# Kernel optimization log

Hardware: AMD Instinct MI355X
Metric: run time of the kernel (lower is better)

## Reference

```python
import jax, jax.numpy as jnp
import numpy as np

MARGIN = 0.3
NORM_EPS = 1e-12  # torch F.normalize default eps


def setup_inputs() -> dict:
    key = jax.random.key(0)
    k1, k2 = jax.random.split(key)
    embeddings = jax.random.normal(k1, (8192, 128), dtype=jnp.float32)
    labels = jax.random.randint(k2, (8192,), 0, 128, dtype=jnp.int64)
    return {"embeddings": embeddings, "labels": labels}


def _triplet_loss(embeddings, labels):
    # L2-normalize rows (torch F.normalize: x / max(||x||, eps))
    norm = jnp.linalg.norm(embeddings, axis=1, keepdims=True)
    e = embeddings / jnp.maximum(norm, NORM_EPS)

    # pairwise squared Euclidean via gram matrix
    dot = e @ e.T                     # [B, B]
    sq = jnp.diagonal(dot)            # [B]
    d2 = jnp.clip(sq[None, :] - 2.0 * dot + sq[:, None], 0.0)
    zmask = (d2 == 0.0).astype(d2.dtype)
    dist = jnp.sqrt(d2 + zmask * 1e-16) * (1.0 - zmask)  # [B, B]

    # hard mining, fully vectorized over rows
    same = labels[:, None] == labels[None, :]
    eye = jnp.eye(labels.shape[0], dtype=bool)
    pos_mask = same & ~eye
    neg_mask = ~same

    dist_ap = jnp.max(jnp.where(pos_mask, dist, -jnp.inf), axis=1)  # hardest positive
    dist_an = jnp.min(jnp.where(neg_mask, dist, jnp.inf), axis=1)   # hardest negative

    valid = pos_mask.any(axis=1) & neg_mask.any(axis=1)
    # MarginRankingLoss(margin)(dist_an, dist_ap, y=1) = mean relu(dist_ap - dist_an + margin)
    per_row = jnp.maximum(dist_ap - dist_an + MARGIN, 0.0)
    n_valid = jnp.maximum(jnp.sum(valid), 1).astype(dist.dtype)
    loss = jnp.sum(jnp.where(valid, per_row, 0.0)) / n_valid
    return jnp.where(valid.any(), loss, jnp.zeros((), dist.dtype))


def reference(embeddings, labels):
    return _triplet_loss(embeddings, labels)
```

## Files before the change

### kernel.cpp

```cpp
#include <hip/hip_runtime.h>
#include <cmath>

#define BN 8192
#define DIM 128
#define MARGIN_F 0.3f
#define NSPLIT 8
#define CPS 1024
#define NT 8
#define NPART (NSPLIT * 2)
#define FBLK 32
#define IMAX 0x7FFFFFFF
#define IMIN 0x80000000

typedef __attribute__((ext_vector_type(4))) int i32x4;

__device__ __forceinline__ int imin3(int a, int b, int c) { return min(a, min(b, c)); }
__device__ __forceinline__ int imax3(int a, int b, int c) { return max(a, max(b, c)); }

__global__ __launch_bounds__(256) void norm_cvt_k(
    const float* __restrict__ emb, float* __restrict__ sqv, unsigned short* __restrict__ EnQ16)
{
  int w = (blockIdx.x * blockDim.x + threadIdx.x) >> 6;
  int lane = threadIdx.x & 63;
  if (w >= BN) return;
  float2 v = *reinterpret_cast<const float2*>(&emb[w * DIM + lane * 2]);
  float s = v.x * v.x + v.y * v.y;
  #pragma unroll
  for (int off = 32; off > 0; off >>= 1) s += __shfl_xor(s, off);
  float iv = 1.0f / fmaxf(sqrtf(s), 1e-12f);
  if (lane == 0) sqv[w] = s * iv * iv;
  int q0 = (int)rintf(127.0f * v.x * iv);
  int q1 = (int)rintf(127.0f * v.y * iv);
  unsigned short us = (unsigned short)((q0 & 255) | ((q1 & 255) << 8));
  int g = lane >> 3;
  EnQ16[(g * BN + w) * 8 + (lane & 7)] = us;
}

__global__ __launch_bounds__(256, 2) void gram_mine_mfma_k(
    const char* __restrict__ EnQ, const int* __restrict__ lab,
    int* __restrict__ ap_part, int* __restrict__ an_part)
{
  __shared__ __align__(16) char Bs[2][16384];

  const int tid = threadIdx.x;
  const int w = tid >> 6, l = tid & 63;
  const int wr = w >> 1, wc = w & 1;
  const int lrow = l & 15, lkg = l >> 4;

  const int rowBase = blockIdx.x * 128 + wr * 64;
  const int panel   = blockIdx.y * CPS;

  i32x4 a[4][2];
  #pragma unroll
  for (int mi = 0; mi < 4; ++mi)
    #pragma unroll
    for (int kk = 0; kk < 2; ++kk)
      a[mi][kk] = *reinterpret_cast<const i32x4*>(
          EnQ + (((size_t)((kk << 2) + lkg) * BN + rowBase + mi * 16 + lrow) << 4));

  unsigned rlbp[4];
  #pragma unroll
  for (int mi = 0; mi < 4; ++mi) {
    int rb = rowBase + mi * 16 + lkg * 4;
    rlbp[mi] = (unsigned)(lab[rb] & 255) | ((unsigned)(lab[rb + 1] & 255) << 8) |
               ((unsigned)(lab[rb + 2] & 255) << 16) | ((unsigned)(lab[rb + 3] & 255) << 24);
  }

  int ap[4][4], an[4][4];
  #pragma unroll
  for (int mi = 0; mi < 4; ++mi)
    #pragma unroll
    for (int r = 0; r < 4; ++r) { ap[mi][r] = IMAX; an[mi][r] = IMIN; }

  auto stage = [&](int buf, int colTile) {
    #pragma unroll
    for (int i = 0; i < 4; ++i) {
      int s0 = (w << 8) + (i << 6);
      int s  = s0 + l;
      const char* gp = EnQ + (((size_t)(s >> 7) * BN + colTile + (s & 127)) << 4);
      __builtin_amdgcn_global_load_lds(
          (const __attribute__((address_space(1))) void*)gp,
          (__attribute__((address_space(3))) void*)(&Bs[buf][s0 * 16]),
          16, 0, 0);
    }
  };

  stage(0, panel);
  __syncthreads();

  int cur = 0;
  #pragma unroll 1
  for (int ct = 0; ct < NT; ++ct) {
    const int colTile = panel + ct * 128;
    const int colBase = colTile + wc * 64;

    if (ct + 1 < NT) stage(cur ^ 1, colTile + 128);

    int clb[4];
    #pragma unroll
    for (int ni = 0; ni < 4; ++ni) clb[ni] = lab[colBase + ni * 16 + lrow];

    const bool diag = (rowBase == colBase);

    #pragma unroll
    for (int half = 0; half < 2; ++half) {
      const int n0 = half * 2, n1 = half * 2 + 1;

      i32x4 acc[4][2] = {};
      #pragma unroll
      for (int kk = 0; kk < 2; ++kk) {
        i32x4 b[2];
        #pragma unroll
        for (int n = 0; n < 2; ++n)
          b[n] = *reinterpret_cast<const i32x4*>(
              &Bs[cur][(((kk << 2) + lkg) * 128 + wc * 64 + (n0 + n) * 16 + lrow) * 16]);
        #pragma unroll
        for (int mi = 0; mi < 4; ++mi)
          #pragma unroll
          for (int n = 0; n < 2; ++n)
            acc[mi][n] = __builtin_amdgcn_mfma_i32_16x16x64_i8(
                a[mi][kk], b[n], acc[mi][n], 0, 0, 0);
      }

      if (diag) {
        #pragma unroll
        for (int mi = 0; mi < 4; ++mi)
          #pragma unroll
          for (int r = 0; r < 4; ++r) {
            int rl = (int)((rlbp[mi] >> (r * 8)) & 255u);
            int rloc = mi * 16 + lkg * 4 + r;
            int d0 = acc[mi][0][r], d1 = acc[mi][1][r];
            bool s0 = (rl == clb[n0]), s1 = (rl == clb[n1]);
            bool e0 = (rloc == n0 * 16 + lrow), e1 = (rloc == n1 * 16 + lrow);
            int p0 = (s0 && !e0) ? d0 : IMAX;
            int p1 = (s1 && !e1) ? d1 : IMAX;
            int q0 = s0 ? IMIN : d0;
            int q1 = s1 ? IMIN : d1;
            ap[mi][r] = imin3(ap[mi][r], p0, p1);
            an[mi][r] = imax3(an[mi][r], q0, q1);
          }
      } else {
        #pragma unroll
        for (int mi = 0; mi < 4; ++mi)
          #pragma unroll
          for (int r = 0; r < 4; ++r) {
            int rl = (int)((rlbp[mi] >> (r * 8)) & 255u);
            int d0 = acc[mi][0][r], d1 = acc[mi][1][r];
            bool s0 = (rl == clb[n0]), s1 = (rl == clb[n1]);
            int p0 = s0 ? d0 : IMAX;
            int p1 = s1 ? d1 : IMAX;
            int q0 = s0 ? IMIN : d0;
            int q1 = s1 ? IMIN : d1;
            ap[mi][r] = imin3(ap[mi][r], p0, p1);
            an[mi][r] = imax3(an[mi][r], q0, q1);
          }
      }
    }

    __syncthreads();
    cur ^= 1;
  }

  const int part = blockIdx.y * 2 + wc;
  #pragma unroll
  for (int mi = 0; mi < 4; ++mi)
    #pragma unroll
    for (int r = 0; r < 4; ++r) {
      int p = ap[mi][r], n = an[mi][r];
      #pragma unroll
      for (int off = 1; off < 16; off <<= 1) {
        p = min(p, __shfl_xor(p, off));
        n = max(n, __shfl_xor(n, off));
      }
      if (lrow == 0) {
        int rg = rowBase + mi * 16 + lkg * 4 + r;
        ap_part[part * BN + rg] = p;
        an_part[part * BN + rg] = n;
      }
    }
}

__global__ __launch_bounds__(256) void finalize_a_k(
    const int* __restrict__ ap_part, const int* __restrict__ an_part,
    const float* __restrict__ sqv,
    float* __restrict__ blk_sum, float* __restrict__ blk_cnt)
{
  int r = blockIdx.x * 256 + threadIdx.x;
  int apt = IMAX, ant = IMIN;
  #pragma unroll 8
  for (int s = 0; s < NPART; ++s) {
    apt = min(apt, ap_part[s * BN + r]);
    ant = max(ant, an_part[s * BN + r]);
  }
  float sum = 0.f, cnt = 0.f;
  if (apt != IMAX && ant != IMIN) {
    const float sc = 2.0f / (127.0f * 127.0f);
    float rs1 = sqv[r] + 1.0f;
    float dap = sqrtf(fmaxf(fmaf(-sc, (float)apt, rs1), 0.f));
    float dan = sqrtf(fmaxf(fmaf(-sc, (float)ant, rs1), 0.f));
    sum = fmaxf(dap - dan + MARGIN_F, 0.f);
    cnt = 1.f;
  }
  #pragma unroll
  for (int off = 32; off > 0; off >>= 1) {
    sum += __shfl_xor(sum, off);
    cnt += __shfl_xor(cnt, off);
  }
  __shared__ float ssum[4], scnt[4];
  int wv = threadIdx.x >> 6;
  if ((threadIdx.x & 63) == 0) { ssum[wv] = sum; scnt[wv] = cnt; }
  __syncthreads();
  if (threadIdx.x == 0) {
    blk_sum[blockIdx.x] = ssum[0] + ssum[1] + ssum[2] + ssum[3];
    blk_cnt[blockIdx.x] = scnt[0] + scnt[1] + scnt[2] + scnt[3];
  }
}

__global__ __launch_bounds__(64) void finalize_b_k(
    const float* __restrict__ blk_sum, const float* __restrict__ blk_cnt,
    float* __restrict__ out)
{
  int l = threadIdx.x;
  float s = (l < FBLK) ? blk_sum[l] : 0.f;
  float c = (l < FBLK) ? blk_cnt[l] : 0.f;
  #pragma unroll
  for (int off = 32; off > 0; off >>= 1) {
    s += __shfl_xor(s, off);
    c += __shfl_xor(c, off);
  }
  if (l == 0) out[0] = (c > 0.f) ? (s / c) : 0.f;
}

extern "C" void kernel_launch(void* const* d_in, const int* in_sizes, int n_in,
                              void* d_out, int out_size, void* d_ws, size_t ws_size,
                              hipStream_t stream)
{
  const float* emb = (const float*)d_in[0];
  const int*   lab = (const int*)d_in[1];
  float* out = (float*)d_out;
  float* ws  = (float*)d_ws;

  float* sqv     = ws;
  int*   ap_part = (int*)(sqv + BN);
  int*   an_part = ap_part + NPART * BN;
  float* blk_sum = (float*)(an_part + NPART * BN);
  float* blk_cnt = blk_sum + FBLK;
  char*  EnQ     = (char*)(blk_cnt + FBLK);

  norm_cvt_k<<<dim3(BN / 4), 256, 0, stream>>>(emb, sqv, (unsigned short*)EnQ);
  gram_mine_mfma_k<<<dim3(BN / 128, NSPLIT), 256, 0, stream>>>(EnQ, lab, ap_part, an_part);
  finalize_a_k<<<dim3(FBLK), 256, 0, stream>>>(ap_part, an_part, sqv, blk_sum, blk_cnt);
  finalize_b_k<<<dim3(1), 64, 0, stream>>>(blk_sum, blk_cnt, out);
}
```

Baseline: 34.09 us.

## Fuse finalize reductions into gram kernel via last-block atomic counters

```diff
diff --git a/kernel.cpp b/kernel.cpp
--- a/kernel.cpp
+++ b/kernel.cpp
@@ -8,7 +8,7 @@
 #define CPS 1024
 #define NT 8
 #define NPART (NSPLIT * 2)
-#define FBLK 32
+#define NRB 64
 #define IMAX 0x7FFFFFFF
 #define IMIN 0x80000000
 
@@ -18,8 +18,11 @@
 __device__ __forceinline__ int imax3(int a, int b, int c) { return max(a, max(b, c)); }
 
 __global__ __launch_bounds__(256) void norm_cvt_k(
-    const float* __restrict__ emb, float* __restrict__ sqv, unsigned short* __restrict__ EnQ16)
+    const float* __restrict__ emb, float* __restrict__ sqv,
+    unsigned short* __restrict__ EnQ16, int* __restrict__ counters)
 {
+  if (blockIdx.x == 0 && threadIdx.x < NRB + 1) counters[threadIdx.x] = 0;
+
   int w = (blockIdx.x * blockDim.x + threadIdx.x) >> 6;
   int lane = threadIdx.x & 63;
   if (w >= BN) return;
@@ -38,9 +41,14 @@
 
 __global__ __launch_bounds__(256, 2) void gram_mine_mfma_k(
     const char* __restrict__ EnQ, const int* __restrict__ lab,
-    int* __restrict__ ap_part, int* __restrict__ an_part)
+    int* __restrict__ ap_part, int* __restrict__ an_part,
+    const float* __restrict__ sqv,
+    float* __restrict__ blk_sum, float* __restrict__ blk_cnt,
+    int* __restrict__ counters, float* __restrict__ out)
 {
   __shared__ __align__(16) char Bs[2][16384];
+  __shared__ int sflag;
+  __shared__ float ssum[4], scnt[4];
 
   const int tid = threadIdx.x;
   const int w = tid >> 6, l = tid & 63;
@@ -178,57 +186,62 @@
         an_part[part * BN + rg] = n;
       }
     }
-}
-
-__global__ __launch_bounds__(256) void finalize_a_k(
-    const int* __restrict__ ap_part, const int* __restrict__ an_part,
-    const float* __restrict__ sqv,
-    float* __restrict__ blk_sum, float* __restrict__ blk_cnt)
-{
-  int r = blockIdx.x * 256 + threadIdx.x;
-  int apt = IMAX, ant = IMIN;
-  #pragma unroll 8
-  for (int s = 0; s < NPART; ++s) {
-    apt = min(apt, ap_part[s * BN + r]);
-    ant = max(ant, an_part[s * BN + r]);
-  }
-  float sum = 0.f, cnt = 0.f;
-  if (apt != IMAX && ant != IMIN) {
-    const float sc = 2.0f / (127.0f * 127.0f);
-    float rs1 = sqv[r] + 1.0f;
-    float dap = sqrtf(fmaxf(fmaf(-sc, (float)apt, rs1), 0.f));
-    float dan = sqrtf(fmaxf(fmaf(-sc, (float)ant, rs1), 0.f));
-    sum = fmaxf(dap - dan + MARGIN_F, 0.f);
-    cnt = 1.f;
+
+  __syncthreads();
+  if (tid == 0) {
+    __threadfence();
+    sflag = (atomicAdd(&counters[blockIdx.x], 1) == NSPLIT - 1);
+  }
+  __syncthreads();
+  if (!sflag) return;
+  __threadfence();
+
+  const int rbase = blockIdx.x * 128;
+  float fsum = 0.f, fcval = 0.f;
+  if (tid < 128) {
+    int r = rbase + tid;
+    int apt = IMAX, ant = IMIN;
+    #pragma unroll 8
+    for (int s = 0; s < NPART; ++s) {
+      apt = min(apt, ap_part[s * BN + r]);
+      ant = max(ant, an_part[s * BN + r]);
+    }
+    if (apt != IMAX && ant != IMIN) {
+      const float sc = 2.0f / (127.0f * 127.0f);
+      float rs1 = sqv[r] + 1.0f;
+      float dap = sqrtf(fmaxf(fmaf(-sc, (float)apt, rs1), 0.f));
+      float dan = sqrtf(fmaxf(fmaf(-sc, (float)ant, rs1), 0.f));
+      fsum = fmaxf(dap - dan + MARGIN_F, 0.f);
+      fcval = 1.f;
+    }
   }
   #pragma unroll
   for (int off = 32; off > 0; off >>= 1) {
-    sum += __shfl_xor(sum, off);
-    cnt += __shfl_xor(cnt, off);
-  }
-  __shared__ float ssum[4], scnt[4];
-  int wv = threadIdx.x >> 6;
-  if ((threadIdx.x & 63) == 0) { ssum[wv] = sum; scnt[wv] = cnt; }
-  __syncthreads();
-  if (threadIdx.x == 0) {
+    fsum  += __shfl_xor(fsum, off);
+    fcval += __shfl_xor(fcval, off);
+  }
+  if ((tid & 63) == 0) { ssum[tid >> 6] = fsum; scnt[tid >> 6] = fcval; }
+  __syncthreads();
+  if (tid == 0) {
     blk_sum[blockIdx.x] = ssum[0] + ssum[1] + ssum[2] + ssum[3];
     blk_cnt[blockIdx.x] = scnt[0] + scnt[1] + scnt[2] + scnt[3];
-  }
-}
-
-__global__ __launch_bounds__(64) void finalize_b_k(
-    const float* __restrict__ blk_sum, const float* __restrict__ blk_cnt,
-    float* __restrict__ out)
-{
-  int l = threadIdx.x;
-  float s = (l < FBLK) ? blk_sum[l] : 0.f;
-  float c = (l < FBLK) ? blk_cnt[l] : 0.f;
-  #pragma unroll
-  for (int off = 32; off > 0; off >>= 1) {
-    s += __shfl_xor(s, off);
-    c += __shfl_xor(c, off);
-  }
-  if (l == 0) out[0] = (c > 0.f) ? (s / c) : 0.f;
+    __threadfence();
+    sflag = (atomicAdd(&counters[NRB], 1) == NRB - 1);
+  }
+  __syncthreads();
+  if (!sflag) return;
+  __threadfence();
+
+  if (tid < 64) {
+    float s = blk_sum[tid], c = blk_cnt[tid];
+    #pragma unroll
+    for (int off = 32; off > 0; off >>= 1) {
+      s += __shfl_xor(s, off);
+      c += __shfl_xor(c, off);
+    }
+    if (tid == 0) out[0] = (c > 0.f) ? (s / c) : 0.f;
+  }
+  if (tid < NRB + 1) counters[tid] = 0;
 }
 
 extern "C" void kernel_launch(void* const* d_in, const int* in_sizes, int n_in,
@@ -240,15 +253,15 @@
   float* out = (float*)d_out;
   float* ws  = (float*)d_ws;
 
-  float* sqv     = ws;
-  int*   ap_part = (int*)(sqv + BN);
-  int*   an_part = ap_part + NPART * BN;
-  float* blk_sum = (float*)(an_part + NPART * BN);
-  float* blk_cnt = blk_sum + FBLK;
-  char*  EnQ     = (char*)(blk_cnt + FBLK);
-
-  norm_cvt_k<<<dim3(BN / 4), 256, 0, stream>>>(emb, sqv, (unsigned short*)EnQ);
-  gram_mine_mfma_k<<<dim3(BN / 128, NSPLIT), 256, 0, stream>>>(EnQ, lab, ap_part, an_part);
-  finalize_a_k<<<dim3(FBLK), 256, 0, stream>>>(ap_part, an_part, sqv, blk_sum, blk_cnt);
-  finalize_b_k<<<dim3(1), 64, 0, stream>>>(blk_sum, blk_cnt, out);
+  float* sqv      = ws;
+  int*   ap_part  = (int*)(sqv + BN);
+  int*   an_part  = ap_part + NPART * BN;
+  float* blk_sum  = (float*)(an_part + NPART * BN);
+  float* blk_cnt  = blk_sum + NRB;
+  int*   counters = (int*)(blk_cnt + NRB);
+  char*  EnQ      = (char*)(counters + NRB + 16);
+
+  norm_cvt_k<<<dim3(BN / 4), 256, 0, stream>>>(emb, sqv, (unsigned short*)EnQ, counters);
+  gram_mine_mfma_k<<<dim3(BN / 128, NSPLIT), 256, 0, stream>>>(
+      EnQ, lab, ap_part, an_part, sqv, blk_sum, blk_cnt, counters, out);
 }
```

Result: slower. 46.46 us (+36.3%).

## Reduce mined distances with atomics and merge finalize into a single kernel

Applied to the files above, without the earlier changes.

```diff
diff --git a/kernel.cpp b/kernel.cpp
--- a/kernel.cpp
+++ b/kernel.cpp
@@ -7,8 +7,6 @@
 #define NSPLIT 8
 #define CPS 1024
 #define NT 8
-#define NPART (NSPLIT * 2)
-#define FBLK 32
 #define IMAX 0x7FFFFFFF
 #define IMIN 0x80000000
 
@@ -18,9 +16,13 @@
 __device__ __forceinline__ int imax3(int a, int b, int c) { return max(a, max(b, c)); }
 
 __global__ __launch_bounds__(256) void norm_cvt_k(
-    const float* __restrict__ emb, float* __restrict__ sqv, unsigned short* __restrict__ EnQ16)
-{
-  int w = (blockIdx.x * blockDim.x + threadIdx.x) >> 6;
+    const float* __restrict__ emb, float* __restrict__ sqv, unsigned short* __restrict__ EnQ16,
+    int* __restrict__ ap_f, int* __restrict__ an_f)
+{
+  int gt = blockIdx.x * blockDim.x + threadIdx.x;
+  if (gt < BN) { ap_f[gt] = IMAX; an_f[gt] = IMIN; }
+
+  int w = gt >> 6;
   int lane = threadIdx.x & 63;
   if (w >= BN) return;
   float2 v = *reinterpret_cast<const float2*>(&emb[w * DIM + lane * 2]);
@@ -38,7 +40,7 @@
 
 __global__ __launch_bounds__(256, 2) void gram_mine_mfma_k(
     const char* __restrict__ EnQ, const int* __restrict__ lab,
-    int* __restrict__ ap_part, int* __restrict__ an_part)
+    int* __restrict__ ap_f, int* __restrict__ an_f)
 {
   __shared__ __align__(16) char Bs[2][16384];
 
@@ -71,6 +73,8 @@
   for (int mi = 0; mi < 4; ++mi)
     #pragma unroll
     for (int r = 0; r < 4; ++r) { ap[mi][r] = IMAX; an[mi][r] = IMIN; }
+
+  const i32x4 zf = {0, 0, 0, 0};
 
   auto stage = [&](int buf, int colTile) {
     #pragma unroll
@@ -106,20 +110,32 @@
     for (int half = 0; half < 2; ++half) {
       const int n0 = half * 2, n1 = half * 2 + 1;
 
-      i32x4 acc[4][2] = {};
-      #pragma unroll
-      for (int kk = 0; kk < 2; ++kk) {
+      i32x4 acc[4][2];
+      {
         i32x4 b[2];
         #pragma unroll
         for (int n = 0; n < 2; ++n)
           b[n] = *reinterpret_cast<const i32x4*>(
-              &Bs[cur][(((kk << 2) + lkg) * 128 + wc * 64 + (n0 + n) * 16 + lrow) * 16]);
+              &Bs[cur][((0 + lkg) * 128 + wc * 64 + (n0 + n) * 16 + lrow) * 16]);
         #pragma unroll
         for (int mi = 0; mi < 4; ++mi)
           #pragma unroll
           for (int n = 0; n < 2; ++n)
             acc[mi][n] = __builtin_amdgcn_mfma_i32_16x16x64_i8(
-                a[mi][kk], b[n], acc[mi][n], 0, 0, 0);
+                a[mi][0], b[n], zf, 0, 0, 0);
+      }
+      {
+        i32x4 b[2];
+        #pragma unroll
+        for (int n = 0; n < 2; ++n)
+          b[n] = *reinterpret_cast<const i32x4*>(
+              &Bs[cur][((4 + lkg) * 128 + wc * 64 + (n0 + n) * 16 + lrow) * 16]);
+        #pragma unroll
+        for (int mi = 0; mi < 4; ++mi)
+          #pragma unroll
+          for (int n = 0; n < 2; ++n)
+            acc[mi][n] = __builtin_amdgcn_mfma_i32_16x16x64_i8(
+                a[mi][1], b[n], acc[mi][n], 0, 0, 0);
       }
 
       if (diag) {
@@ -161,7 +177,6 @@
     cur ^= 1;
   }
 
-  const int part = blockIdx.y * 2 + wc;
   #pragma unroll
   for (int mi = 0; mi < 4; ++mi)
     #pragma unroll
@@ -174,61 +189,46 @@
       }
       if (lrow == 0) {
         int rg = rowBase + mi * 16 + lkg * 4 + r;
-        ap_part[part * BN + rg] = p;
-        an_part[part * BN + rg] = n;
-      }
-    }
-}
-
-__global__ __launch_bounds__(256) void finalize_a_k(
-    const int* __restrict__ ap_part, const int* __restrict__ an_part,
-    const float* __restrict__ sqv,
-    float* __restrict__ blk_sum, float* __restrict__ blk_cnt)
-{
-  int r = blockIdx.x * 256 + threadIdx.x;
-  int apt = IMAX, ant = IMIN;
-  #pragma unroll 8
-  for (int s = 0; s < NPART; ++s) {
-    apt = min(apt, ap_part[s * BN + r]);
-    ant = max(ant, an_part[s * BN + r]);
-  }
+        atomicMin(&ap_f[rg], p);
+        atomicMax(&an_f[rg], n);
+      }
+    }
+}
+
+__global__ __launch_bounds__(1024) void finalize_k(
+    const int* __restrict__ ap_f, const int* __restrict__ an_f,
+    const float* __restrict__ sqv, float* __restrict__ out)
+{
+  int t = threadIdx.x;
   float sum = 0.f, cnt = 0.f;
-  if (apt != IMAX && ant != IMIN) {
-    const float sc = 2.0f / (127.0f * 127.0f);
-    float rs1 = sqv[r] + 1.0f;
-    float dap = sqrtf(fmaxf(fmaf(-sc, (float)apt, rs1), 0.f));
-    float dan = sqrtf(fmaxf(fmaf(-sc, (float)ant, rs1), 0.f));
-    sum = fmaxf(dap - dan + MARGIN_F, 0.f);
-    cnt = 1.f;
+  #pragma unroll
+  for (int i = 0; i < BN / 1024; ++i) {
+    int r = i * 1024 + t;
+    int apt = ap_f[r], ant = an_f[r];
+    if (apt != IMAX && ant != IMIN) {
+      const float sc = 2.0f / (127.0f * 127.0f);
+      float rs1 = sqv[r] + 1.0f;
+      float dap = sqrtf(fmaxf(fmaf(-sc, (float)apt, rs1), 0.f));
+      float dan = sqrtf(fmaxf(fmaf(-sc, (float)ant, rs1), 0.f));
+      sum += fmaxf(dap - dan + MARGIN_F, 0.f);
+      cnt += 1.f;
+    }
   }
   #pragma unroll
   for (int off = 32; off > 0; off >>= 1) {
     sum += __shfl_xor(sum, off);
     cnt += __shfl_xor(cnt, off);
   }
-  __shared__ float ssum[4], scnt[4];
-  int wv = threadIdx.x >> 6;
-  if ((threadIdx.x & 63) == 0) { ssum[wv] = sum; scnt[wv] = cnt; }
+  __shared__ float ssum[16], scnt[16];
+  int wv = t >> 6;
+  if ((t & 63) == 0) { ssum[wv] = sum; scnt[wv] = cnt; }
   __syncthreads();
-  if (threadIdx.x == 0) {
-    blk_sum[blockIdx.x] = ssum[0] + ssum[1] + ssum[2] + ssum[3];
-    blk_cnt[blockIdx.x] = scnt[0] + scnt[1] + scnt[2] + scnt[3];
-  }
-}
-
-__global__ __launch_bounds__(64) void finalize_b_k(
-    const float* __restrict__ blk_sum, const float* __restrict__ blk_cnt,
-    float* __restrict__ out)
-{
-  int l = threadIdx.x;
-  float s = (l < FBLK) ? blk_sum[l] : 0.f;
-  float c = (l < FBLK) ? blk_cnt[l] : 0.f;
-  #pragma unroll
-  for (int off = 32; off > 0; off >>= 1) {
-    s += __shfl_xor(s, off);
-    c += __shfl_xor(c, off);
-  }
-  if (l == 0) out[0] = (c > 0.f) ? (s / c) : 0.f;
+  if (t == 0) {
+    float s = 0.f, c = 0.f;
+    #pragma unroll
+    for (int i = 0; i < 16; ++i) { s += ssum[i]; c += scnt[i]; }
+    out[0] = (c > 0.f) ? (s / c) : 0.f;
+  }
 }
 
 extern "C" void kernel_launch(void* const* d_in, const int* in_sizes, int n_in,
@@ -240,15 +240,12 @@
   float* out = (float*)d_out;
   float* ws  = (float*)d_ws;
 
-  float* sqv     = ws;
-  int*   ap_part = (int*)(sqv + BN);
-  int*   an_part = ap_part + NPART * BN;
-  float* blk_sum = (float*)(an_part + NPART * BN);
-  float* blk_cnt = blk_sum + FBLK;
-  char*  EnQ     = (char*)(blk_cnt + FBLK);
-
-  norm_cvt_k<<<dim3(BN / 4), 256, 0, stream>>>(emb, sqv, (unsigned short*)EnQ);
-  gram_mine_mfma_k<<<dim3(BN / 128, NSPLIT), 256, 0, stream>>>(EnQ, lab, ap_part, an_part);
-  finalize_a_k<<<dim3(FBLK), 256, 0, stream>>>(ap_part, an_part, sqv, blk_sum, blk_cnt);
-  finalize_b_k<<<dim3(1), 64, 0, stream>>>(blk_sum, blk_cnt, out);
-}
+  float* sqv  = ws;
+  int*   ap_f = (int*)(sqv + BN);
+  int*   an_f = ap_f + BN;
+  char*  EnQ  = (char*)(an_f + BN);
+
+  norm_cvt_k<<<dim3(BN / 4), 256, 0, stream>>>(emb, sqv, (unsigned short*)EnQ, ap_f, an_f);
+  gram_mine_mfma_k<<<dim3(BN / 128, NSPLIT), 256, 0, stream>>>(EnQ, lab, ap_f, an_f);
+  finalize_k<<<dim3(1), 1024, 0, stream>>>(ap_f, an_f, sqv, out);
+}
```

New measurement: 35.82 us. 5.0% more time.
